# Performance work log

Measured on AMD Instinct MI355X. Metric: run time of the kernel, lower is better.

## Reference

```python
import jax, jax.numpy as jnp
import numpy as np

S, N, M = 8, 4096, 64          # snapshots, atoms, total neighbors (sum of max_num_neighs)
L = 20.0                        # periodic box length
R_CS, R_C = 2.0, 6.0            # smooth cutoff radii
DSUB = 16                       # dim_sub_net
PAD_FRAC = 0.15                 # fraction of -1 padded neighbor slots


def _mlp(x, params):
    # DenseChainNet: Linear -> relu between layers, no activation after last layer
    n = len(params)
    for i, (W, b) in enumerate(params):
        x = x @ W + b
        if i < n - 1:
            x = jax.nn.relu(x)
    return x


def _lin(k, fan_in, fan_out):
    k1, k2 = jax.random.split(k)
    s = 1.0 / np.sqrt(fan_in)
    W = jax.random.uniform(k1, (fan_in, fan_out), minval=-s, maxval=s, dtype=jnp.float32)
    b = jax.random.uniform(k2, (fan_out,), minval=-s, maxval=s, dtype=jnp.float32)
    return W, b


def setup_inputs() -> dict:
    key = jax.random.key(0)
    ks = jax.random.split(key, 12)
    inputs = jax.random.uniform(ks[0], (S, N, 3), dtype=jnp.float32) * L
    input_types = jax.random.randint(ks[1], (S, N), 0, 2)
    # neighbor indices, guaranteed != self, with -1 padding
    base = jnp.arange(N, dtype=jnp.int32)[None, :, None]
    off = jax.random.randint(ks[2], (S, N, M), 1, N)
    neigh = (base + off) % N
    pad = jax.random.uniform(ks[3], (S, N, M)) < PAD_FRAC
    neigh_list = jnp.where(pad, -1, neigh).astype(jnp.int32)
    es1_w, es1_b = _lin(ks[4], 2, 4)
    es2_w, es2_b = _lin(ks[5], 4, 4)
    fs1_w, fs1_b = _lin(ks[6], 4, 4)
    fs2_w, fs2_b = _lin(ks[7], 4, 4)
    en1_w, en1_b = _lin(ks[8], 4, 8)
    en2_w, en2_b = _lin(ks[9], 8, 16)
    en3_w, en3_b = _lin(ks[10], 16, 32)
    return dict(inputs=inputs, input_types=input_types, neigh_list=neigh_list,
                es1_w=es1_w, es1_b=es1_b, es2_w=es2_w, es2_b=es2_b,
                fs1_w=fs1_w, fs1_b=fs1_b, fs2_w=fs2_w, fs2_b=fs2_b,
                en1_w=en1_w, en1_b=en1_b, en2_w=en2_w, en2_b=en2_b,
                en3_w=en3_w, en3_b=en3_b)


def reference(inputs, input_types, neigh_list,
              es1_w, es1_b, es2_w, es2_b,
              fs1_w, fs1_b, fs2_w, fs2_b,
              en1_w, en1_b, en2_w, en2_b, en3_w, en3_b):
    mask = neigh_list == -1                               # [S,N,M]
    idx = jnp.where(mask, 0, neigh_list)
    flat = idx.reshape(S, N * M)
    # gather neighbor coordinates with periodic minimum-image convention
    pos_j = jnp.take_along_axis(inputs, flat[..., None], axis=1).reshape(S, N, M, 3)
    d = pos_j - inputs[:, :, None, :]
    d = d - L * jnp.round(d / L)
    r = jnp.sqrt(jnp.sum(d * d, axis=-1) + 1e-12)         # [S,N,M]
    # smooth cutoff: s(r) = 1/r for r<r_cs, cosine switch to 0 at r_c
    u = (r - R_CS) / (R_C - R_CS)
    sw = jnp.where(r < R_CS, 1.0,
                   jnp.where(r < R_C, 0.5 * jnp.cos(jnp.pi * u) + 0.5, 0.0))
    s_ij = jnp.where(mask, 0.0, sw / r)                   # [S,N,M]
    r_ij = d * (s_ij / r)[..., None]                      # s(r) * d / r, [S,N,M,3]
    # species pair descriptor (symmetrized over pair order)
    neigh_types = jnp.take_along_axis(input_types, flat, axis=1).reshape(S, N, M)
    self_t = jnp.broadcast_to(input_types[:, :, None], (S, N, M))
    pairs = jnp.stack([self_t, neigh_types], axis=-1).astype(jnp.float32).reshape(-1, 2)
    es = [(es1_w, es1_b), (es2_w, es2_b)]
    td = _mlp(pairs, es) + _mlp(pairs[:, ::-1], es)
    td = _mlp(td, [(fs1_w, fs1_b), (fs2_w, fs2_b)]).reshape(S, N, M, -1)  # [S,N,M,4]
    s_tilde = (td * s_ij[..., None]).reshape(S * N * M, -1)
    G = _mlp(s_tilde, [(en1_w, en1_b), (en2_w, en2_b), (en3_w, en3_b)]).reshape(S, N, M, -1)  # [S,N,M,32]
    r_tilde = jnp.concatenate([s_ij[..., None], r_ij], axis=-1)            # [S,N,M,4]
    R = jnp.einsum('snmd,snmk->sndk', r_tilde, G[..., :DSUB])              # [S,N,4,16]
    R1 = jnp.einsum('snmd,sndk->snmk', r_tilde, R)                         # [S,N,M,16]
    D = jnp.einsum('snmg,snmk->sngk', G, R1)                               # [S,N,32,16]
    return D
```

## Files before the change

### kernel.cpp

```cpp
#include <hip/hip_runtime.h>
#include <math.h>

#define SS 8
#define NN 4096
#define MM 64
#define LBOX 20.0f

typedef __attribute__((ext_vector_type(8)))  short    short8;
typedef __attribute__((ext_vector_type(2)))  float    floatx2;
typedef __attribute__((ext_vector_type(4)))  float    floatx4;
typedef __attribute__((ext_vector_type(2)))  __bf16   bf16x2;

__device__ inline unsigned pkbf(float a, float b) {
    bf16x2 p; p.x = (__bf16)a; p.y = (__bf16)b;
    unsigned u; __builtin_memcpy(&u, &p, 4); return u;
}

#define WS_POSW   0
#define WS_WT     (524288 / 4)
#define WT_VT     0
#define WT_B3P    32
#define WT_W3P    64

__global__ __launch_bounds__(256) void prep_kernel(
    const float* __restrict__ pos, const int* __restrict__ types,
    const float* __restrict__ es1_w, const float* __restrict__ es1_b,
    const float* __restrict__ es2_w, const float* __restrict__ es2_b,
    const float* __restrict__ fs1_w, const float* __restrict__ fs1_b,
    const float* __restrict__ fs2_w, const float* __restrict__ fs2_b,
    const float* __restrict__ en1_w, const float* __restrict__ en3_w,
    const float* __restrict__ en3_b, float* __restrict__ ws)
{
    const int tid = threadIdx.x;
    const int b = blockIdx.x;
    if (b < 128) {
        const int i = b * 256 + tid;
        floatx4 v;
        v.x = pos[i * 3 + 0];
        v.y = pos[i * 3 + 1];
        v.z = pos[i * 3 + 2];
        v.w = __int_as_float(types[i]);
        *((floatx4*)ws + i) = v;
        return;
    }
    float* wt = ws + WS_WT;
    if (tid < 4) {
        const float ti = (float)(tid >> 1), tj = (float)(tid & 1);
        float e[4] = {0.f, 0.f, 0.f, 0.f};
        #pragma unroll
        for (int swp = 0; swp < 2; ++swp) {
            const float a = swp ? tj : ti, bb = swp ? ti : tj;
            float h[4];
            #pragma unroll
            for (int k = 0; k < 4; ++k)
                h[k] = fmaxf(a * es1_w[k] + bb * es1_w[4 + k] + es1_b[k], 0.f);
            #pragma unroll
            for (int k = 0; k < 4; ++k) {
                float acc = es2_b[k];
                #pragma unroll
                for (int j = 0; j < 4; ++j) acc += h[j] * es2_w[j * 4 + k];
                e[k] += acc;
            }
        }
        float f[4];
        #pragma unroll
        for (int k = 0; k < 4; ++k) {
            float acc = fs1_b[k];
            #pragma unroll
            for (int j = 0; j < 4; ++j) acc += e[j] * fs1_w[j * 4 + k];
            f[k] = fmaxf(acc, 0.f);
        }
        float td[4];
        #pragma unroll
        for (int k = 0; k < 4; ++k) {
            float acc = fs2_b[k];
            #pragma unroll
            for (int j = 0; j < 4; ++j) acc += f[j] * fs2_w[j * 4 + k];
            td[k] = acc;
        }
        #pragma unroll
        for (int o = 0; o < 8; ++o) {
            float acc = 0.f;
            #pragma unroll
            for (int d = 0; d < 4; ++d) acc += td[d] * en1_w[d * 8 + o];
            wt[WT_VT + tid * 8 + o] = acc;
        }
    }
    if (tid < 32)
        wt[WT_B3P + tid] = en3_b[(tid & 1) * 16 + (tid >> 1)];
    #pragma unroll
    for (int rr = 0; rr < 2; ++rr) {
        const int i = tid + rr * 256;
        const int hp = i >> 6, g = (i >> 2) & 15, w = i & 3;
        wt[WT_W3P + i] = en3_w[(2 * hp + (w >> 1)) * 32 + g + 16 * (w & 1)];
    }
}

__global__ __launch_bounds__(256) void desc_kernel(
    const float* __restrict__ ws,
    const int*   __restrict__ neigh,
    const float* __restrict__ en1_b,
    const float* __restrict__ en2_w, const float* __restrict__ en2_b,
    float* __restrict__ out)
{
    __shared__ alignas(16) unsigned short sh_h2[4][16][72];
    __shared__ alignas(16) unsigned short sh_rt[4][4][72];
    __shared__ alignas(16) float sh_PT[4][4][20];
    __shared__ alignas(16) float sh_W3p[512];
    __shared__ alignas(16) float sh_b3p[16][2];
    __shared__ alignas(16) float sh_A[4][128];
    __shared__ alignas(16) float sh_vt[4][8];

    const int tid = threadIdx.x;
    const float* wt = ws + WS_WT;

    if (tid < 32) {
        ((float*)sh_vt)[tid]  = wt[WT_VT + tid];
        ((float*)sh_b3p)[tid] = wt[WT_B3P + tid];
    }
    sh_W3p[tid]       = wt[WT_W3P + tid];
    sh_W3p[tid + 256] = wt[WT_W3P + 256 + tid];
    __syncthreads();

    const int wave = __builtin_amdgcn_readfirstlane(tid >> 6);
    const int lane = tid & 63;
    const int atom = __builtin_amdgcn_readfirstlane(blockIdx.x * 4 + (tid >> 6));
    const int sbase = atom & ~(NN - 1);
    const floatx4* __restrict__ pw = (const floatx4*)ws;

    const floatx4 pi4 = pw[atom];
    const float xi = pi4.x, yi = pi4.y, zi = pi4.z;
    const int   ti = __float_as_int(pi4.w);

    const int nb  = neigh[atom * MM + lane];
    const int msk = nb < 0;
    const int gj  = sbase + (msk ? 0 : nb);
    const floatx4 pj4 = pw[gj];
    const int tj = __float_as_int(pj4.w);

    float dx = pj4.x - xi;
    float dy = pj4.y - yi;
    float dz = pj4.z - zi;
    dx -= LBOX * rintf(dx * (1.0f / LBOX));
    dy -= LBOX * rintf(dy * (1.0f / LBOX));
    dz -= LBOX * rintf(dz * (1.0f / LBOX));
    const float r2   = fmaf(dx, dx, fmaf(dy, dy, fmaf(dz, dz, 1e-12f)));
    const float rinv = rsqrtf(r2);
    const float r    = r2 * rinv;
    const float u    = fminf(fmaxf((r - 2.0f) * 0.25f, 0.0f), 1.0f);
    const float swv  = 0.5f * __cosf(3.14159265358979323846f * u) + 0.5f;
    const float sij   = msk ? 0.0f : swv * rinv;
    const float scale = sij * rinv;
    const int   tt    = ti * 2 + tj;

    const floatx2 zero2 = {0.f, 0.f};
    const floatx2 sij2  = {sij, sij};
    float h1[8];
    #pragma unroll
    for (int j = 0; j < 4; ++j) {
        const floatx2 vtp = *(const floatx2*)&sh_vt[tt][j * 2];
        const floatx2 ebp = *(const floatx2*)&en1_b[j * 2];
        floatx2 hp = sij2 * vtp + ebp;
        hp = __builtin_elementwise_max(hp, zero2);
        h1[j * 2]     = hp.x;
        h1[j * 2 + 1] = hp.y;
    }

    {
        floatx2 acc[8];
        #pragma unroll
        for (int kp = 0; kp < 8; ++kp)
            acc[kp] = *(const floatx2*)&en2_b[kp * 2];
        #pragma unroll
        for (int i = 0; i < 8; ++i) {
            const floatx2 hi = {h1[i], h1[i]};
            #pragma unroll
            for (int kp = 0; kp < 8; ++kp)
                acc[kp] += hi * (*(const floatx2*)&en2_w[i * 16 + kp * 2]);
        }
        #pragma unroll
        for (int kp = 0; kp < 8; ++kp) {
            const floatx2 a = __builtin_elementwise_max(acc[kp], zero2);
            const unsigned pk = pkbf(a.x, a.y);
            sh_h2[wave][kp * 2][lane]     = (unsigned short)pk;
            sh_h2[wave][kp * 2 + 1][lane] = (unsigned short)(pk >> 16);
        }
    }
    {
        const unsigned p0 = pkbf(sij, dx * scale), p1 = pkbf(dy * scale, dz * scale);
        sh_rt[wave][0][lane] = (unsigned short)p0;
        sh_rt[wave][1][lane] = (unsigned short)(p0 >> 16);
        sh_rt[wave][2][lane] = (unsigned short)p1;
        sh_rt[wave][3][lane] = (unsigned short)(p1 >> 16);
    }
    asm volatile("s_waitcnt lgkmcnt(0)" ::: "memory");

    const int col16 = lane & 15;
    const int q4    = lane >> 4;
    const int m0    = q4 * 8;
    floatx4 cP = {0.f, 0.f, 0.f, 0.f};
    floatx4 cQ = {0.f, 0.f, 0.f, 0.f};
    const short8 ones = (short8)(short)0x3F80;
    #pragma unroll
    for (int ck = 0; ck < 2; ++ck) {
        const short8 af = *(const short8*)&sh_h2[wave][col16][ck * 32 + m0];
        const short8 bf = *(const short8*)&sh_rt[wave][col16 & 3][ck * 32 + m0];
        cP = __builtin_amdgcn_mfma_f32_16x16x32_bf16(af, bf, cP, 0, 0, 0);
        cQ = __builtin_amdgcn_mfma_f32_16x16x32_bf16(ones, bf, cQ, 0, 0, 0);
    }
    if (col16 < 4) *(floatx4*)&sh_PT[wave][col16][q4 * 4] = cP;
    const float qd = cQ[0];
    asm volatile("s_waitcnt lgkmcnt(0)" ::: "memory");

    {
        const int g0 = lane >> 2, dd = lane & 3;
        const floatx2 b3v = *(const floatx2*)&sh_b3p[g0][0];
        floatx2 acc2 = floatx2{qd, qd} * b3v;
        #pragma unroll
        for (int h4 = 0; h4 < 4; ++h4) {
            const floatx4 pv = *(const floatx4*)&sh_PT[wave][dd][h4 * 4];
            const floatx4 wa = *(const floatx4*)&sh_W3p[(h4 * 2 + 0) * 64 + g0 * 4];
            const floatx4 wb = *(const floatx4*)&sh_W3p[(h4 * 2 + 1) * 64 + g0 * 4];
            acc2 += floatx2{pv.x, pv.x} * floatx2{wa.x, wa.y};
            acc2 += floatx2{pv.y, pv.y} * floatx2{wa.z, wa.w};
            acc2 += floatx2{pv.z, pv.z} * floatx2{wb.x, wb.y};
            acc2 += floatx2{pv.w, pv.w} * floatx2{wb.z, wb.w};
        }
        sh_A[wave][lane]      = acc2.x;
        sh_A[wave][lane + 64] = acc2.y;
    }
    asm volatile("s_waitcnt lgkmcnt(0)" ::: "memory");

    {
        const int g = lane >> 1, koff = (lane & 1) * 8;
        const floatx4 Ag = *(const floatx4*)&sh_A[wave][g * 4];
        floatx4 o0, o1;
        #pragma unroll
        for (int jj = 0; jj < 8; ++jj) {
            const floatx4 Ak = *(const floatx4*)&sh_A[wave][(koff + jj) * 4];
            const float v = fmaf(Ag.x, Ak.x, fmaf(Ag.y, Ak.y, fmaf(Ag.z, Ak.z, Ag.w * Ak.w)));
            if (jj < 4) o0[jj] = v; else o1[jj - 4] = v;
        }
        float* op = out + (size_t)atom * 512 + lane * 8;
        __builtin_nontemporal_store(o0, (floatx4*)op);
        __builtin_nontemporal_store(o1, (floatx4*)(op + 4));
    }
}

extern "C" void kernel_launch(void* const* d_in, const int* in_sizes, int n_in,
                              void* d_out, int out_size, void* d_ws, size_t ws_size,
                              hipStream_t stream) {
    const float* pos   = (const float*)d_in[0];
    const int*   typ   = (const int*)d_in[1];
    const int*   ngh   = (const int*)d_in[2];
    float* ws = (float*)d_ws;

    prep_kernel<<<dim3(129), dim3(256), 0, stream>>>(
        pos, typ,
        (const float*)d_in[3],  (const float*)d_in[4],
        (const float*)d_in[5],  (const float*)d_in[6],
        (const float*)d_in[7],  (const float*)d_in[8],
        (const float*)d_in[9],  (const float*)d_in[10],
        (const float*)d_in[11],
        (const float*)d_in[15], (const float*)d_in[16],
        ws);

    desc_kernel<<<dim3((SS * NN) / 4), dim3(256), 0, stream>>>(
        ws, ngh,
        (const float*)d_in[12],
        (const float*)d_in[13], (const float*)d_in[14],
        (float*)d_out);
}
```

Before: 125.8 us.

## Fuse prep kernel into descriptor kernel and gather positions directly

Removes the separate prep kernel that packed positions and types into a float4 workspace and precomputed the small type-MLP table and permuted en3 weights. Each descriptor block now computes the type table and weight permutation itself, and neighbor positions are read straight from the xyz array with an unaligned 16-byte load plus a separate types load, clamped at the array end. This saves one kernel launch and the round trip through the workspace. In exchange every block redoes the tiny weight prep, and each neighbor gather now issues two loads that are not 16-byte aligned instead of one aligned load.

```diff
diff --git a/kernel.cpp b/kernel.cpp
--- a/kernel.cpp
+++ b/kernel.cpp
@@ -9,6 +9,7 @@
 typedef __attribute__((ext_vector_type(8)))  short    short8;
 typedef __attribute__((ext_vector_type(2)))  float    floatx2;
 typedef __attribute__((ext_vector_type(4)))  float    floatx4;
+typedef __attribute__((ext_vector_type(4), aligned(4))) float floatx4u;
 typedef __attribute__((ext_vector_type(2)))  __bf16   bf16x2;
 
 __device__ inline unsigned pkbf(float a, float b) {
@@ -16,91 +17,16 @@
     unsigned u; __builtin_memcpy(&u, &p, 4); return u;
 }
 
-#define WS_POSW   0
-#define WS_WT     (524288 / 4)
-#define WT_VT     0
-#define WT_B3P    32
-#define WT_W3P    64
-
-__global__ __launch_bounds__(256) void prep_kernel(
+__global__ __launch_bounds__(256) void desc_kernel(
     const float* __restrict__ pos, const int* __restrict__ types,
+    const int*   __restrict__ neigh,
     const float* __restrict__ es1_w, const float* __restrict__ es1_b,
     const float* __restrict__ es2_w, const float* __restrict__ es2_b,
     const float* __restrict__ fs1_w, const float* __restrict__ fs1_b,
     const float* __restrict__ fs2_w, const float* __restrict__ fs2_b,
-    const float* __restrict__ en1_w, const float* __restrict__ en3_w,
-    const float* __restrict__ en3_b, float* __restrict__ ws)
-{
-    const int tid = threadIdx.x;
-    const int b = blockIdx.x;
-    if (b < 128) {
-        const int i = b * 256 + tid;
-        floatx4 v;
-        v.x = pos[i * 3 + 0];
-        v.y = pos[i * 3 + 1];
-        v.z = pos[i * 3 + 2];
-        v.w = __int_as_float(types[i]);
-        *((floatx4*)ws + i) = v;
-        return;
-    }
-    float* wt = ws + WS_WT;
-    if (tid < 4) {
-        const float ti = (float)(tid >> 1), tj = (float)(tid & 1);
-        float e[4] = {0.f, 0.f, 0.f, 0.f};
-        #pragma unroll
-        for (int swp = 0; swp < 2; ++swp) {
-            const float a = swp ? tj : ti, bb = swp ? ti : tj;
-            float h[4];
-            #pragma unroll
-            for (int k = 0; k < 4; ++k)
-                h[k] = fmaxf(a * es1_w[k] + bb * es1_w[4 + k] + es1_b[k], 0.f);
-            #pragma unroll
-            for (int k = 0; k < 4; ++k) {
-                float acc = es2_b[k];
-                #pragma unroll
-                for (int j = 0; j < 4; ++j) acc += h[j] * es2_w[j * 4 + k];
-                e[k] += acc;
-            }
-        }
-        float f[4];
-        #pragma unroll
-        for (int k = 0; k < 4; ++k) {
-            float acc = fs1_b[k];
-            #pragma unroll
-            for (int j = 0; j < 4; ++j) acc += e[j] * fs1_w[j * 4 + k];
-            f[k] = fmaxf(acc, 0.f);
-        }
-        float td[4];
-        #pragma unroll
-        for (int k = 0; k < 4; ++k) {
-            float acc = fs2_b[k];
-            #pragma unroll
-            for (int j = 0; j < 4; ++j) acc += f[j] * fs2_w[j * 4 + k];
-            td[k] = acc;
-        }
-        #pragma unroll
-        for (int o = 0; o < 8; ++o) {
-            float acc = 0.f;
-            #pragma unroll
-            for (int d = 0; d < 4; ++d) acc += td[d] * en1_w[d * 8 + o];
-            wt[WT_VT + tid * 8 + o] = acc;
-        }
-    }
-    if (tid < 32)
-        wt[WT_B3P + tid] = en3_b[(tid & 1) * 16 + (tid >> 1)];
-    #pragma unroll
-    for (int rr = 0; rr < 2; ++rr) {
-        const int i = tid + rr * 256;
-        const int hp = i >> 6, g = (i >> 2) & 15, w = i & 3;
-        wt[WT_W3P + i] = en3_w[(2 * hp + (w >> 1)) * 32 + g + 16 * (w & 1)];
-    }
-}
-
-__global__ __launch_bounds__(256) void desc_kernel(
-    const float* __restrict__ ws,
-    const int*   __restrict__ neigh,
-    const float* __restrict__ en1_b,
+    const float* __restrict__ en1_w, const float* __restrict__ en1_b,
     const float* __restrict__ en2_w, const float* __restrict__ en2_b,
+    const float* __restrict__ en3_w, const float* __restrict__ en3_b,
     float* __restrict__ out)
 {
     __shared__ alignas(16) unsigned short sh_h2[4][16][72];
@@ -112,35 +38,85 @@
     __shared__ alignas(16) float sh_vt[4][8];
 
     const int tid = threadIdx.x;
-    const float* wt = ws + WS_WT;
-
-    if (tid < 32) {
-        ((float*)sh_vt)[tid]  = wt[WT_VT + tid];
-        ((float*)sh_b3p)[tid] = wt[WT_B3P + tid];
-    }
-    sh_W3p[tid]       = wt[WT_W3P + tid];
-    sh_W3p[tid + 256] = wt[WT_W3P + 256 + tid];
+
+    if (tid < 4) {
+        const float ti = (float)(tid >> 1), tj = (float)(tid & 1);
+        float e[4] = {0.f, 0.f, 0.f, 0.f};
+        #pragma unroll
+        for (int swp = 0; swp < 2; ++swp) {
+            const float a = swp ? tj : ti, bb = swp ? ti : tj;
+            float h[4];
+            #pragma unroll
+            for (int k = 0; k < 4; ++k)
+                h[k] = fmaxf(a * es1_w[k] + bb * es1_w[4 + k] + es1_b[k], 0.f);
+            #pragma unroll
+            for (int k = 0; k < 4; ++k) {
+                float acc = es2_b[k];
+                #pragma unroll
+                for (int j = 0; j < 4; ++j) acc += h[j] * es2_w[j * 4 + k];
+                e[k] += acc;
+            }
+        }
+        float f[4];
+        #pragma unroll
+        for (int k = 0; k < 4; ++k) {
+            float acc = fs1_b[k];
+            #pragma unroll
+            for (int j = 0; j < 4; ++j) acc += e[j] * fs1_w[j * 4 + k];
+            f[k] = fmaxf(acc, 0.f);
+        }
+        float td[4];
+        #pragma unroll
+        for (int k = 0; k < 4; ++k) {
+            float acc = fs2_b[k];
+            #pragma unroll
+            for (int j = 0; j < 4; ++j) acc += f[j] * fs2_w[j * 4 + k];
+            td[k] = acc;
+        }
+        #pragma unroll
+        for (int o = 0; o < 8; ++o) {
+            float acc = 0.f;
+            #pragma unroll
+            for (int d = 0; d < 4; ++d) acc += td[d] * en1_w[d * 8 + o];
+            sh_vt[tid][o] = acc;
+        }
+    }
+    if (tid < 32)
+        ((float*)sh_b3p)[tid] = en3_b[(tid & 1) * 16 + (tid >> 1)];
+    #pragma unroll
+    for (int rr = 0; rr < 2; ++rr) {
+        const int i = tid + rr * 256;
+        const int hp = i >> 6, g = (i >> 2) & 15, w = i & 3;
+        sh_W3p[i] = en3_w[(2 * hp + (w >> 1)) * 32 + g + 16 * (w & 1)];
+    }
     __syncthreads();
 
     const int wave = __builtin_amdgcn_readfirstlane(tid >> 6);
     const int lane = tid & 63;
     const int atom = __builtin_amdgcn_readfirstlane(blockIdx.x * 4 + (tid >> 6));
     const int sbase = atom & ~(NN - 1);
-    const floatx4* __restrict__ pw = (const floatx4*)ws;
-
-    const floatx4 pi4 = pw[atom];
-    const float xi = pi4.x, yi = pi4.y, zi = pi4.z;
-    const int   ti = __float_as_int(pi4.w);
+
+    const float xi = pos[atom * 3 + 0];
+    const float yi = pos[atom * 3 + 1];
+    const float zi = pos[atom * 3 + 2];
+    const int   ti = types[atom];
 
     const int nb  = neigh[atom * MM + lane];
     const int msk = nb < 0;
-    const int gj  = sbase + (msk ? 0 : nb);
-    const floatx4 pj4 = pw[gj];
-    const int tj = __float_as_int(pj4.w);
-
-    float dx = pj4.x - xi;
-    float dy = pj4.y - yi;
-    float dz = pj4.z - zi;
+    const int ja  = sbase + (msk ? 0 : nb);
+    const int ja3 = ja * 3;
+    const int shft = (ja3 + 4 > SS * NN * 3);
+    const int ja3c = shft ? ja3 - 1 : ja3;
+    floatx4u pv4;
+    __builtin_memcpy(&pv4, pos + ja3c, 16);
+    const float pjx = shft ? pv4.y : pv4.x;
+    const float pjy = shft ? pv4.z : pv4.y;
+    const float pjz = shft ? pv4.w : pv4.z;
+    const int   tj  = types[ja];
+
+    float dx = pjx - xi;
+    float dy = pjy - yi;
+    float dz = pjz - zi;
     dx -= LBOX * rintf(dx * (1.0f / LBOX));
     dy -= LBOX * rintf(dy * (1.0f / LBOX));
     dz -= LBOX * rintf(dz * (1.0f / LBOX));
@@ -250,24 +226,14 @@
 extern "C" void kernel_launch(void* const* d_in, const int* in_sizes, int n_in,
                               void* d_out, int out_size, void* d_ws, size_t ws_size,
                               hipStream_t stream) {
-    const float* pos   = (const float*)d_in[0];
-    const int*   typ   = (const int*)d_in[1];
-    const int*   ngh   = (const int*)d_in[2];
-    float* ws = (float*)d_ws;
-
-    prep_kernel<<<dim3(129), dim3(256), 0, stream>>>(
-        pos, typ,
+    desc_kernel<<<dim3((SS * NN) / 4), dim3(256), 0, stream>>>(
+        (const float*)d_in[0],  (const int*)d_in[1],  (const int*)d_in[2],
         (const float*)d_in[3],  (const float*)d_in[4],
         (const float*)d_in[5],  (const float*)d_in[6],
         (const float*)d_in[7],  (const float*)d_in[8],
         (const float*)d_in[9],  (const float*)d_in[10],
-        (const float*)d_in[11],
+        (const float*)d_in[11], (const float*)d_in[12],
+        (const float*)d_in[13], (const float*)d_in[14],
         (const float*)d_in[15], (const float*)d_in[16],
-        ws);
-
-    desc_kernel<<<dim3((SS * NN) / 4), dim3(256), 0, stream>>>(
-        ws, ngh,
-        (const float*)d_in[12],
-        (const float*)d_in[13], (const float*)d_in[14],
         (float*)d_out);
 }
```

Result: slower. 130.2 us (+3.4%).
